# Kernel tuning notes

Hardware: AMD Instinct MI355X
Metric: run time of the kernel (lower is better)

The kernel has to match this reference:

```python
import jax, jax.numpy as jnp
import numpy as np


def setup_inputs() -> dict:
    key = jax.random.key(0)
    k_x, k_w = jax.random.split(key)
    B, Din, T, K = 256, 128, 2000, 64
    x_in = jax.random.normal(k_x, (B, Din, T), dtype=jnp.float32)
    W = 0.1 * jax.random.normal(k_w, (K, Din), dtype=jnp.float32)
    bias = jnp.zeros((K,), dtype=jnp.float32)
    vth = jnp.ones((K,), dtype=jnp.float32)
    tau = jnp.linspace(8.0, 25.0, K, dtype=jnp.float32)  # tau_ms buffer default
    return {"x_in": x_in, "W": W, "bias": bias, "vth": vth, "tau": tau}


def reference(x_in, W, bias, vth, tau):
    B, Din, T = x_in.shape
    K = W.shape[0]
    alpha = jnp.exp(-1.0 / tau)  # [K]

    # Precompute input currents for all timesteps in one GEMM: [T, B, K]
    I_all = jnp.einsum('bdt,kd->tbk', x_in, W) + bias

    def step(V, I_t):
        # V: [B, K] membrane potential carried across time
        V = alpha * V + I_t
        S = (V - vth > 0).astype(V.dtype)  # hard threshold spike
        V = V - S * vth                    # soft reset
        return V, (S, V)

    V0 = jnp.zeros((B, K), dtype=x_in.dtype)
    _, (S_hist, V_hist) = jax.lax.scan(step, V0, I_all)
    # [T, B, K] -> [B, K, T]
    S_hist = jnp.transpose(S_hist, (1, 2, 0))
    V_hist = jnp.transpose(V_hist, (1, 2, 0))
    return (S_hist, V_hist)
```

## Files before the change

kernel.cpp:

```cpp
#include <hip/hip_runtime.h>

#define B_SZ   256
#define DIN    128
#define T_LEN  2000
#define K_SZ   64
#define TT     64
#define NTILE  32
#define ISTR   68

__device__ __forceinline__ void stage_load(const float* __restrict__ xl, float4 (&st)[8]) {
#pragma unroll
  for (int q = 0; q < 8; ++q)
    st[q] = *(const float4*)(xl + (size_t)q * 4 * T_LEN);
}

__device__ __forceinline__ void stage_write(float* __restrict__ Xb, const float4 (&st)[8],
                                            int wave, int lane) {
  float* base = Xb + (wave * 32 + (lane >> 4)) * TT + (lane & 15) * 4;
#pragma unroll
  for (int q = 0; q < 8; ++q)
    *(float4*)(base + q * 4 * TT) = st[q];
}

__device__ __forceinline__ void gemm_range(const float* __restrict__ Xb,
                                           const float* __restrict__ Wt,
                                           int d0, int d1, int i4, int j4,
                                           float (&acc)[16]) {
#pragma unroll 4
  for (int d = d0; d < d1; ++d) {
    const float4 w4 = *(const float4*)&Wt[d * K_SZ + i4];
    const float4 x4 = *(const float4*)&Xb[d * TT + j4];
    acc[0]  = fmaf(w4.x, x4.x, acc[0]);  acc[1]  = fmaf(w4.x, x4.y, acc[1]);
    acc[2]  = fmaf(w4.x, x4.z, acc[2]);  acc[3]  = fmaf(w4.x, x4.w, acc[3]);
    acc[4]  = fmaf(w4.y, x4.x, acc[4]);  acc[5]  = fmaf(w4.y, x4.y, acc[5]);
    acc[6]  = fmaf(w4.y, x4.z, acc[6]);  acc[7]  = fmaf(w4.y, x4.w, acc[7]);
    acc[8]  = fmaf(w4.z, x4.x, acc[8]);  acc[9]  = fmaf(w4.z, x4.y, acc[9]);
    acc[10] = fmaf(w4.z, x4.z, acc[10]); acc[11] = fmaf(w4.z, x4.w, acc[11]);
    acc[12] = fmaf(w4.w, x4.x, acc[12]); acc[13] = fmaf(w4.w, x4.y, acc[13]);
    acc[14] = fmaf(w4.w, x4.z, acc[14]); acc[15] = fmaf(w4.w, x4.w, acc[15]);
  }
}

__device__ __forceinline__ void writeI(float* __restrict__ Iw, const float (&acc)[16],
                                       int i4, int j4) {
#pragma unroll
  for (int mi = 0; mi < 4; ++mi)
    *(float4*)&Iw[(i4 + mi) * ISTR + j4] =
        make_float4(acc[4*mi], acc[4*mi+1], acc[4*mi+2], acc[4*mi+3]);
}

__device__ __forceinline__ void scan16(const float* __restrict__ Ir, int c0, int tg,
                                       float bias_s, float alpha, float vth_s,
                                       float& V, float* __restrict__ outS,
                                       float* __restrict__ outV, int sk, bool active)
{
#pragma unroll
  for (int q = 0; q < 4; ++q) {
    const float4 iv = *(const float4*)&Ir[c0 + 4*q];
    float S0,S1,S2,S3, V0,V1,V2,V3;
    { const float Vp = fmaf(alpha, V, iv.x + bias_s); const bool sp = Vp > vth_s;
      V0 = sp ? (Vp - vth_s) : Vp; S0 = sp ? 1.0f : 0.0f; V = V0; }
    { const float Vp = fmaf(alpha, V, iv.y + bias_s); const bool sp = Vp > vth_s;
      V1 = sp ? (Vp - vth_s) : Vp; S1 = sp ? 1.0f : 0.0f; V = V1; }
    { const float Vp = fmaf(alpha, V, iv.z + bias_s); const bool sp = Vp > vth_s;
      V2 = sp ? (Vp - vth_s) : Vp; S2 = sp ? 1.0f : 0.0f; V = V2; }
    { const float Vp = fmaf(alpha, V, iv.w + bias_s); const bool sp = Vp > vth_s;
      V3 = sp ? (Vp - vth_s) : Vp; S3 = sp ? 1.0f : 0.0f; V = V3; }
    if (active) {
      *(float4*)&outS[(size_t)sk * T_LEN + tg + 4*q] = make_float4(S0, S1, S2, S3);
      *(float4*)&outV[(size_t)sk * T_LEN + tg + 4*q] = make_float4(V0, V1, V2, V3);
    }
  }
}

__global__ __launch_bounds__(256, 1)
void lif_fused(const float* __restrict__ x,
               const float* __restrict__ W,
               const float* __restrict__ bias,
               const float* __restrict__ vth,
               const float* __restrict__ tau,
               float* __restrict__ out)
{
  __shared__ __align__(16) float Wt[DIN * K_SZ];
  __shared__ __align__(16) float Xt[2][DIN * TT];
  __shared__ __align__(16) float Ibuf[2][K_SZ * ISTR];

  const int tid  = threadIdx.x;
  const int b    = blockIdx.x;
  const int wave = tid >> 6;
  const int lane = tid & 63;
  const int i4   = (tid >> 4) << 2;
  const int j4   = (tid & 15) << 2;

  for (int idx = tid; idx < DIN * K_SZ; idx += 256) {
    const int k = idx >> 7;
    const int d = idx & 127;
    Wt[d * K_SZ + k] = W[idx];
  }

  const int   sk     = (wave << 4) + (lane & 15);
  const float alpha  = expf(-1.0f / tau[sk]);
  const float vth_s  = vth[sk];
  const float bias_s = bias[sk];

  const float* xb   = x + (size_t)b * (DIN * T_LEN);
  float*       outS = out + (size_t)b * (K_SZ * T_LEN);
  float*       outV = outS + (size_t)B_SZ * K_SZ * T_LEN;

  const float* xl = xb + (size_t)(32 * wave + (lane >> 4)) * T_LEN + (lane & 15) * 4;

  const bool active = (lane < 16);
  float V = 0.0f;
  float acc[16];
  float4 st[8];

  stage_load(xl + 0, st);
  stage_write(Xt[0], st, wave, lane);
  __syncthreads();

  {
    stage_load(xl + 64, st);
#pragma unroll
    for (int i = 0; i < 16; ++i) acc[i] = 0.0f;
    gemm_range(Xt[0], Wt, 0, 64, i4, j4, acc);
    stage_write(Xt[1], st, wave, lane);
    gemm_range(Xt[0], Wt, 64, 128, i4, j4, acc);
    writeI(Ibuf[0], acc, i4, j4);
    __syncthreads();
  }

#pragma unroll 1
  for (int tile = 1; tile <= 30; ++tile) {
    const int cur = tile & 1;
    const float* Xc = Xt[cur];
    float*       Xn = Xt[cur ^ 1];
    float*       Iw = Ibuf[cur];
    const float* Ir = Ibuf[cur ^ 1] + (size_t)sk * ISTR;
    const int   tp0 = (tile - 1) * 64;
    const int  st0n = (tile + 1 == NTILE - 1) ? (T_LEN - TT) : (tile + 1) * 64;

    stage_load(xl + st0n, st);
#pragma unroll
    for (int i = 0; i < 16; ++i) acc[i] = 0.0f;

    gemm_range(Xc, Wt, 0, 64, i4, j4, acc);
    scan16(Ir,  0, tp0 +  0, bias_s, alpha, vth_s, V, outS, outV, sk, active);
    scan16(Ir, 16, tp0 + 16, bias_s, alpha, vth_s, V, outS, outV, sk, active);
    stage_write(Xn, st, wave, lane);
    gemm_range(Xc, Wt, 64, 128, i4, j4, acc);
    scan16(Ir, 32, tp0 + 32, bias_s, alpha, vth_s, V, outS, outV, sk, active);
    scan16(Ir, 48, tp0 + 48, bias_s, alpha, vth_s, V, outS, outV, sk, active);
    writeI(Iw, acc, i4, j4);
    __syncthreads();
  }

  {
    const float* Xc = Xt[1];
    const float* Ir = Ibuf[0] + (size_t)sk * ISTR;
    const int   tp0 = 30 * 64;
#pragma unroll
    for (int i = 0; i < 16; ++i) acc[i] = 0.0f;
    gemm_range(Xc, Wt, 0, 64, i4, j4, acc);
    scan16(Ir,  0, tp0 +  0, bias_s, alpha, vth_s, V, outS, outV, sk, active);
    scan16(Ir, 16, tp0 + 16, bias_s, alpha, vth_s, V, outS, outV, sk, active);
    gemm_range(Xc, Wt, 64, 128, i4, j4, acc);
    scan16(Ir, 32, tp0 + 32, bias_s, alpha, vth_s, V, outS, outV, sk, active);
    scan16(Ir, 48, tp0 + 48, bias_s, alpha, vth_s, V, outS, outV, sk, active);
    writeI(Ibuf[1], acc, i4, j4);
  }

  {
    const float* Ir = Ibuf[1] + (size_t)sk * ISTR;
    scan16(Ir, 48, 1984, bias_s, alpha, vth_s, V, outS, outV, sk, active);
  }
}

extern "C" void kernel_launch(void* const* d_in, const int* in_sizes, int n_in,
                              void* d_out, int out_size, void* d_ws, size_t ws_size,
                              hipStream_t stream) {
  const float* x    = (const float*)d_in[0];
  const float* W    = (const float*)d_in[1];
  const float* bias = (const float*)d_in[2];
  const float* vth  = (const float*)d_in[3];
  const float* tau  = (const float*)d_in[4];
  float* out        = (float*)d_out;

  lif_fused<<<dim3(B_SZ), dim3(256), 0, stream>>>(x, W, bias, vth, tau, out);
}
```

Measured before the change: 593.6 us.

## Stream x directly from global and drop LDS staging and block barriers

Removes the LDS double-buffered x tiles and the in-kernel W transpose. A separate kernel now pre-transposes W into workspace. Each lane reads its own time column of x straight from global memory, and each wave computes 16 output channels, reading W through wave-uniform scalar loads. The tile loop now needs no __syncthreads, because each wave only scans the rows of the I buffer it wrote itself. In exchange, every x element is loaded four times (once per wave) through the caches, the GEMM and scan no longer overlap across phases, and there is an extra kernel launch.

```diff
diff --git a/kernel.cpp b/kernel.cpp
--- a/kernel.cpp
+++ b/kernel.cpp
@@ -8,45 +8,13 @@
 #define NTILE  32
 #define ISTR   68
 
-__device__ __forceinline__ void stage_load(const float* __restrict__ xl, float4 (&st)[8]) {
-#pragma unroll
-  for (int q = 0; q < 8; ++q)
-    st[q] = *(const float4*)(xl + (size_t)q * 4 * T_LEN);
-}
-
-__device__ __forceinline__ void stage_write(float* __restrict__ Xb, const float4 (&st)[8],
-                                            int wave, int lane) {
-  float* base = Xb + (wave * 32 + (lane >> 4)) * TT + (lane & 15) * 4;
-#pragma unroll
-  for (int q = 0; q < 8; ++q)
-    *(float4*)(base + q * 4 * TT) = st[q];
-}
-
-__device__ __forceinline__ void gemm_range(const float* __restrict__ Xb,
-                                           const float* __restrict__ Wt,
-                                           int d0, int d1, int i4, int j4,
-                                           float (&acc)[16]) {
-#pragma unroll 4
-  for (int d = d0; d < d1; ++d) {
-    const float4 w4 = *(const float4*)&Wt[d * K_SZ + i4];
-    const float4 x4 = *(const float4*)&Xb[d * TT + j4];
-    acc[0]  = fmaf(w4.x, x4.x, acc[0]);  acc[1]  = fmaf(w4.x, x4.y, acc[1]);
-    acc[2]  = fmaf(w4.x, x4.z, acc[2]);  acc[3]  = fmaf(w4.x, x4.w, acc[3]);
-    acc[4]  = fmaf(w4.y, x4.x, acc[4]);  acc[5]  = fmaf(w4.y, x4.y, acc[5]);
-    acc[6]  = fmaf(w4.y, x4.z, acc[6]);  acc[7]  = fmaf(w4.y, x4.w, acc[7]);
-    acc[8]  = fmaf(w4.z, x4.x, acc[8]);  acc[9]  = fmaf(w4.z, x4.y, acc[9]);
-    acc[10] = fmaf(w4.z, x4.z, acc[10]); acc[11] = fmaf(w4.z, x4.w, acc[11]);
-    acc[12] = fmaf(w4.w, x4.x, acc[12]); acc[13] = fmaf(w4.w, x4.y, acc[13]);
-    acc[14] = fmaf(w4.w, x4.z, acc[14]); acc[15] = fmaf(w4.w, x4.w, acc[15]);
+__global__ void transpose_w(const float* __restrict__ W, float* __restrict__ Wt) {
+  const int idx = blockIdx.x * 256 + threadIdx.x;
+  if (idx < K_SZ * DIN) {
+    const int k = idx >> 7;
+    const int d = idx & 127;
+    Wt[d * K_SZ + k] = W[idx];
   }
-}
-
-__device__ __forceinline__ void writeI(float* __restrict__ Iw, const float (&acc)[16],
-                                       int i4, int j4) {
-#pragma unroll
-  for (int mi = 0; mi < 4; ++mi)
-    *(float4*)&Iw[(i4 + mi) * ISTR + j4] =
-        make_float4(acc[4*mi], acc[4*mi+1], acc[4*mi+2], acc[4*mi+3]);
 }
 
 __device__ __forceinline__ void scan16(const float* __restrict__ Ir, int c0, int tg,
@@ -75,30 +43,21 @@
 
 __global__ __launch_bounds__(256, 1)
 void lif_fused(const float* __restrict__ x,
-               const float* __restrict__ W,
+               const float* __restrict__ Wt,
                const float* __restrict__ bias,
                const float* __restrict__ vth,
                const float* __restrict__ tau,
                float* __restrict__ out)
 {
-  __shared__ __align__(16) float Wt[DIN * K_SZ];
-  __shared__ __align__(16) float Xt[2][DIN * TT];
   __shared__ __align__(16) float Ibuf[2][K_SZ * ISTR];
 
   const int tid  = threadIdx.x;
   const int b    = blockIdx.x;
-  const int wave = tid >> 6;
+  const int wave = __builtin_amdgcn_readfirstlane(tid >> 6);
   const int lane = tid & 63;
-  const int i4   = (tid >> 4) << 2;
-  const int j4   = (tid & 15) << 2;
+  const int k0   = wave << 4;
 
-  for (int idx = tid; idx < DIN * K_SZ; idx += 256) {
-    const int k = idx >> 7;
-    const int d = idx & 127;
-    Wt[d * K_SZ + k] = W[idx];
-  }
-
-  const int   sk     = (wave << 4) + (lane & 15);
+  const int   sk     = k0 + (lane & 15);
   const float alpha  = expf(-1.0f / tau[sk]);
   const float vth_s  = vth[sk];
   const float bias_s = bias[sk];
@@ -107,71 +66,56 @@
   float*       outS = out + (size_t)b * (K_SZ * T_LEN);
   float*       outV = outS + (size_t)B_SZ * K_SZ * T_LEN;
 
-  const float* xl = xb + (size_t)(32 * wave + (lane >> 4)) * T_LEN + (lane & 15) * 4;
-
   const bool active = (lane < 16);
   float V = 0.0f;
   float acc[16];
-  float4 st[8];
-
-  stage_load(xl + 0, st);
-  stage_write(Xt[0], st, wave, lane);
-  __syncthreads();
-
-  {
-    stage_load(xl + 64, st);
-#pragma unroll
-    for (int i = 0; i < 16; ++i) acc[i] = 0.0f;
-    gemm_range(Xt[0], Wt, 0, 64, i4, j4, acc);
-    stage_write(Xt[1], st, wave, lane);
-    gemm_range(Xt[0], Wt, 64, 128, i4, j4, acc);
-    writeI(Ibuf[0], acc, i4, j4);
-    __syncthreads();
-  }
 
 #pragma unroll 1
-  for (int tile = 1; tile <= 30; ++tile) {
-    const int cur = tile & 1;
-    const float* Xc = Xt[cur];
-    float*       Xn = Xt[cur ^ 1];
-    float*       Iw = Ibuf[cur];
-    const float* Ir = Ibuf[cur ^ 1] + (size_t)sk * ISTR;
-    const int   tp0 = (tile - 1) * 64;
-    const int  st0n = (tile + 1 == NTILE - 1) ? (T_LEN - TT) : (tile + 1) * 64;
+  for (int tile = 0; tile < NTILE; ++tile) {
+    const int t0 = tile * TT;
+    int tcol = t0 + lane;
+    if (tcol > T_LEN - 1) tcol = T_LEN - 1;
+    const float* xcol = xb + tcol;
 
-    stage_load(xl + st0n, st);
 #pragma unroll
     for (int i = 0; i < 16; ++i) acc[i] = 0.0f;
 
-    gemm_range(Xc, Wt, 0, 64, i4, j4, acc);
-    scan16(Ir,  0, tp0 +  0, bias_s, alpha, vth_s, V, outS, outV, sk, active);
-    scan16(Ir, 16, tp0 + 16, bias_s, alpha, vth_s, V, outS, outV, sk, active);
-    stage_write(Xn, st, wave, lane);
-    gemm_range(Xc, Wt, 64, 128, i4, j4, acc);
-    scan16(Ir, 32, tp0 + 32, bias_s, alpha, vth_s, V, outS, outV, sk, active);
-    scan16(Ir, 48, tp0 + 48, bias_s, alpha, vth_s, V, outS, outV, sk, active);
-    writeI(Iw, acc, i4, j4);
-    __syncthreads();
+#pragma unroll 4
+    for (int d = 0; d < DIN; ++d) {
+      const float xv = xcol[(size_t)d * T_LEN];
+      const float* wp = Wt + d * K_SZ + k0;
+      const float4 w0 = *(const float4*)(wp + 0);
+      const float4 w1 = *(const float4*)(wp + 4);
+      const float4 w2 = *(const float4*)(wp + 8);
+      const float4 w3 = *(const float4*)(wp + 12);
+      acc[0]  = fmaf(w0.x, xv, acc[0]);  acc[1]  = fmaf(w0.y, xv, acc[1]);
+      acc[2]  = fmaf(w0.z, xv, acc[2]);  acc[3]  = fmaf(w0.w, xv, acc[3]);
+      acc[4]  = fmaf(w1.x, xv, acc[4]);  acc[5]  = fmaf(w1.y, xv, acc[5]);
+      acc[6]  = fmaf(w1.z, xv, acc[6]);  acc[7]  = fmaf(w1.w, xv, acc[7]);
+      acc[8]  = fmaf(w2.x, xv, acc[8]);  acc[9]  = fmaf(w2.y, xv, acc[9]);
+      acc[10] = fmaf(w2.z, xv, acc[10]); acc[11] = fmaf(w2.w, xv, acc[11]);
+      acc[12] = fmaf(w3.x, xv, acc[12]); acc[13] = fmaf(w3.y, xv, acc[13]);
+      acc[14] = fmaf(w3.z, xv, acc[14]); acc[15] = fmaf(w3.w, xv, acc[15]);
+    }
+
+    float* Iw = Ibuf[tile & 1];
+#pragma unroll
+    for (int kk = 0; kk < 16; ++kk)
+      Iw[(k0 + kk) * ISTR + lane] = acc[kk];
+
+    if (tile > 0) {
+      const float* Ir = Ibuf[(tile - 1) & 1] + (size_t)sk * ISTR;
+      const int   tp0 = (tile - 1) * TT;
+      scan16(Ir,  0, tp0 +  0, bias_s, alpha, vth_s, V, outS, outV, sk, active);
+      scan16(Ir, 16, tp0 + 16, bias_s, alpha, vth_s, V, outS, outV, sk, active);
+      scan16(Ir, 32, tp0 + 32, bias_s, alpha, vth_s, V, outS, outV, sk, active);
+      scan16(Ir, 48, tp0 + 48, bias_s, alpha, vth_s, V, outS, outV, sk, active);
+    }
   }
 
   {
-    const float* Xc = Xt[1];
-    const float* Ir = Ibuf[0] + (size_t)sk * ISTR;
-    const int   tp0 = 30 * 64;
-#pragma unroll
-    for (int i = 0; i < 16; ++i) acc[i] = 0.0f;
-    gemm_range(Xc, Wt, 0, 64, i4, j4, acc);
-    scan16(Ir,  0, tp0 +  0, bias_s, alpha, vth_s, V, outS, outV, sk, active);
-    scan16(Ir, 16, tp0 + 16, bias_s, alpha, vth_s, V, outS, outV, sk, active);
-    gemm_range(Xc, Wt, 64, 128, i4, j4, acc);
-    scan16(Ir, 32, tp0 + 32, bias_s, alpha, vth_s, V, outS, outV, sk, active);
-    scan16(Ir, 48, tp0 + 48, bias_s, alpha, vth_s, V, outS, outV, sk, active);
-    writeI(Ibuf[1], acc, i4, j4);
-  }
-
-  {
-    const float* Ir = Ibuf[1] + (size_t)sk * ISTR;
-    scan16(Ir, 48, 1984, bias_s, alpha, vth_s, V, outS, outV, sk, active);
+    const float* Ir = Ibuf[(NTILE - 1) & 1] + (size_t)sk * ISTR;
+    scan16(Ir, 0, (NTILE - 1) * TT, bias_s, alpha, vth_s, V, outS, outV, sk, active);
   }
 }
 
@@ -184,6 +128,8 @@
   const float* vth  = (const float*)d_in[3];
   const float* tau  = (const float*)d_in[4];
   float* out        = (float*)d_out;
+  float* Wt         = (float*)d_ws;
 
-  lif_fused<<<dim3(B_SZ), dim3(256), 0, stream>>>(x, W, bias, vth, tau, out);
+  transpose_w<<<dim3((K_SZ * DIN + 255) / 256), dim3(256), 0, stream>>>(W, Wt);
+  lif_fused<<<dim3(B_SZ), dim3(256), 0, stream>>>(x, Wt, bias, vth, tau, out);
 }
```

Measured after the change: 1.020 ms. 71.8% more time.
